# Optimization experiments

Measured on AMD Instinct MI355X. Metric: run time of the kernel, lower is better.

Reference implementation:

```python
import jax, jax.numpy as jnp
import numpy as np

NUM_USERS = 100_000
NUM_ITEMS = 50_000
DIM = 64
N_INTERACTIONS = 2_000_000  # symmetric nnz = 4M


def setup_inputs() -> dict:
    rng = np.random.default_rng(0)
    u = rng.integers(0, NUM_USERS, N_INTERACTIONS)
    it = rng.integers(0, NUM_ITEMS, N_INTERACTIONS) + NUM_USERS  # items offset by num_users
    rows = np.concatenate([u, it]).astype(np.int32)  # symmetric adjacency
    cols = np.concatenate([it, u]).astype(np.int32)
    n_nodes = NUM_USERS + NUM_ITEMS
    deg = np.bincount(rows, minlength=n_nodes).astype(np.float32)
    deg = np.maximum(deg, 1.0)
    # LightGCN symmetric normalization: A_hat[i,j] = 1/sqrt(deg_i * deg_j)
    vals = (1.0 / np.sqrt(deg[rows] * deg[cols])).astype(np.float32)

    key = jax.random.key(0)
    k1, k2 = jax.random.split(key)
    user_emb = jax.random.normal(k1, (NUM_USERS, DIM), jnp.float32) * 0.1
    item_emb = jax.random.normal(k2, (NUM_ITEMS, DIM), jnp.float32) * 0.1
    return {
        "user_emb": user_emb,
        "item_emb": item_emb,
        "rows": jnp.asarray(rows),
        "cols": jnp.asarray(cols),
        "vals": jnp.asarray(vals),
        "n_layers": 3,
    }


def reference(user_emb, item_emb, rows, cols, vals, n_layers):
    num_users = user_emb.shape[0]
    n_nodes = num_users + item_emb.shape[0]
    emb = jnp.concatenate([user_emb, item_emb], axis=0)  # [N, D]
    acc = emb
    cur = emb
    for _ in range(n_layers):
        # SpMM: cur = A_hat @ cur, via edge gather + weighted segment reduction
        msgs = vals[:, None] * cur[cols]  # [nnz, D]
        cur = jax.ops.segment_sum(msgs, rows, num_segments=n_nodes)
        acc = acc + cur
    all_emb = acc / (n_layers + 1)  # mean over [e0, e1, ..., eL]
    return all_emb[:num_users], all_emb[num_users:]
```

## Files before the change

### kernel.cpp

```cpp
#include <hip/hip_runtime.h>
#include <hip/hip_fp16.h>

#define D 64
#define NLAYERS 3
#define CHUNK 8192
#define RPB 256
#define NBMAX 640
#define NCHMAX 512
#define STAGE_CAP 8704

__global__ void init_concat(const float* __restrict__ ue, const float* __restrict__ ie,
                            const float* __restrict__ invsq,
                            __half* __restrict__ w0, float* __restrict__ acc,
                            int n_user_elems, int n_total_elems) {
    int i4 = (blockIdx.x * blockDim.x + threadIdx.x) * 4;
    if (i4 >= n_total_elems) return;
    float4 v;
    if (i4 < n_user_elems) v = *(const float4*)(ue + i4);
    else                   v = *(const float4*)(ie + (i4 - n_user_elems));
    *(float4*)(acc + i4) = v;
    float isr = invsq[i4 >> 6];
    __half2 h01 = __floats2half2_rn(isr * v.x, isr * v.y);
    __half2 h23 = __floats2half2_rn(isr * v.z, isr * v.w);
    float2 packed;
    *(__half2*)&packed.x = h01;
    *(__half2*)&packed.y = h23;
    *(float2*)(w0 + i4) = packed;
}

__global__ void partition_edges(const int* __restrict__ rows, const int* __restrict__ cols,
                                int* __restrict__ gsorted, int* __restrict__ goff_c,
                                int nnz, int nb) {
    __shared__ int staged[CHUNK];
    __shared__ int cnt[NBMAX];
    __shared__ int cur[NBMAX];
    __shared__ int partial[256];
    int t = threadIdx.x;
    int base = blockIdx.x * CHUNK;

    for (int j = t; j <= nb; j += 256) cnt[j] = 0;
    __syncthreads();
    for (int k = 0; k < CHUNK; k += 256) {
        int e = base + k + t;
        if (e < nnz) atomicAdd(&cnt[rows[e] >> 8], 1);
    }
    __syncthreads();
    int i0 = t * 3, i1 = i0 + 1, i2 = i0 + 2;
    int v0 = (i0 < nb) ? cnt[i0] : 0;
    int v1 = (i1 < nb) ? cnt[i1] : 0;
    int v2 = (i2 < nb) ? cnt[i2] : 0;
    partial[t] = v0 + v1 + v2;
    __syncthreads();
    for (int off = 1; off < 256; off <<= 1) {
        int x = (t >= off) ? partial[t - off] : 0;
        __syncthreads();
        partial[t] += x;
        __syncthreads();
    }
    int excl = (t == 0) ? 0 : partial[t - 1];
    if (i0 <= nb) cnt[i0] = excl;
    if (i1 <= nb) cnt[i1] = excl + v0;
    if (i2 <= nb) cnt[i2] = excl + v0 + v1;
    __syncthreads();
    for (int j = t; j < nb; j += 256) cur[j] = cnt[j];
    __syncthreads();
    for (int k = 0; k < CHUNK; k += 256) {
        int e = base + k + t;
        if (e < nnz) {
            int r = rows[e];
            int pos = atomicAdd(&cur[r >> 8], 1);
            staged[pos] = ((r & 255) << 18) | cols[e];
        }
    }
    __syncthreads();
    int total = cnt[nb];
    for (int i = t; i < total; i += 256) gsorted[base + i] = staged[i];
    for (int j = t; j <= nb; j += 256) goff_c[blockIdx.x * (nb + 1) + j] = cnt[j];
}

__global__ void transpose_off(const int* __restrict__ goff_c, int* __restrict__ T,
                              int nch, int nbp1) {
    int c = blockIdx.x * 256 + threadIdx.x;
    int j = blockIdx.y;
    if (c < nch) T[j * nch + c] = goff_c[c * nbp1 + j];
}

__global__ void bucket_totals(const int* __restrict__ T, int* __restrict__ btot, int nch) {
    int b = blockIdx.x;
    int lane = threadIdx.x;
    int s = 0;
    for (int c = lane; c < nch; c += 64)
        s += T[(size_t)(b + 1) * nch + c] - T[(size_t)b * nch + c];
    for (int off = 32; off; off >>= 1) s += __shfl_down(s, off, 64);
    if (lane == 0) btot[b] = s;
}

__global__ void scan_buckets(const int* __restrict__ btot, int* __restrict__ bb,
                             int* __restrict__ rp, int nb, int n_nodes, int nnz) {
    __shared__ int partial[256];
    int t = threadIdx.x;
    int i0 = t * 3, i1 = i0 + 1, i2 = i0 + 2;
    int v0 = (i0 < nb) ? btot[i0] : 0;
    int v1 = (i1 < nb) ? btot[i1] : 0;
    int v2 = (i2 < nb) ? btot[i2] : 0;
    partial[t] = v0 + v1 + v2;
    __syncthreads();
    for (int off = 1; off < 256; off <<= 1) {
        int x = (t >= off) ? partial[t - off] : 0;
        __syncthreads();
        partial[t] += x;
        __syncthreads();
    }
    int excl = (t == 0) ? 0 : partial[t - 1];
    if (i0 <= nb) bb[i0] = excl;
    if (i1 <= nb) bb[i1] = excl + v0;
    if (i2 <= nb) bb[i2] = excl + v0 + v1;
    if (t == 0) rp[n_nodes] = nnz;
}

__global__ __launch_bounds__(256)
void csr_build_bucket(const int* __restrict__ T, const int* __restrict__ gsorted,
                      const int* __restrict__ bb,
                      int* __restrict__ rp, float* __restrict__ invsq,
                      int* __restrict__ ci, int nch, int n_nodes) {
    __shared__ int staged[STAGE_CAP];
    __shared__ int sbeg[NCHMAX];
    __shared__ int slen[NCHMAX];
    __shared__ int soff[NCHMAX];
    __shared__ int cnt[RPB];
    __shared__ int cursor[RPB];
    __shared__ int scanb[256];
    int t = threadIdx.x;
    int b = blockIdx.x;
    for (int j = t; j < nch; j += 256) {
        int s0 = T[(size_t)b * nch + j];
        int s1 = T[(size_t)(b + 1) * nch + j];
        sbeg[j] = s0;
        slen[j] = s1 - s0;
    }
    cnt[t] = 0;
    __syncthreads();
    int i0 = 2 * t, i1 = 2 * t + 1;
    int l0 = (i0 < nch) ? slen[i0] : 0;
    int l1 = (i1 < nch) ? slen[i1] : 0;
    scanb[t] = l0 + l1;
    __syncthreads();
    for (int off = 1; off < 256; off <<= 1) {
        int x = (t >= off) ? scanb[t - off] : 0;
        __syncthreads();
        scanb[t] += x;
        __syncthreads();
    }
    int texcl = scanb[t] - (l0 + l1);
    if (i0 < nch) soff[i0] = texcl;
    if (i1 < nch) soff[i1] = texcl + l0;
    int total = scanb[255];
    __syncthreads();

    int w = t >> 6, lane = t & 63;
    int sub = lane >> 4, l16 = lane & 15;
    bool fits = (total <= STAGE_CAP);
    if (fits) {
        for (int c = (w << 2) + sub; c < nch; c += 16) {
            const int* seg = gsorted + (size_t)c * CHUNK + sbeg[c];
            int L = slen[c], o = soff[c];
            for (int i = l16; i < L; i += 16) staged[o + i] = seg[i];
        }
        __syncthreads();
        for (int i = t; i < total; i += 256) atomicAdd(&cnt[staged[i] >> 18], 1);
    } else {
        for (int c = (w << 2) + sub; c < nch; c += 16) {
            const int* seg = gsorted + (size_t)c * CHUNK + sbeg[c];
            int L = slen[c];
            for (int i = l16; i < L; i += 16) atomicAdd(&cnt[seg[i] >> 18], 1);
        }
    }
    __syncthreads();
    int v = cnt[t];
    scanb[t] = v;
    __syncthreads();
    for (int off = 1; off < 256; off <<= 1) {
        int x = (t >= off) ? scanb[t - off] : 0;
        __syncthreads();
        scanb[t] += x;
        __syncthreads();
    }
    int excl = scanb[t] - v;
    int base = bb[b];
    int grow = (b << 8) + t;
    if (grow < n_nodes) {
        rp[grow] = base + excl;
        float d = (float)v;
        invsq[grow] = rsqrtf(d < 1.f ? 1.f : d);
    }
    cursor[t] = base + excl;
    __syncthreads();
    if (fits) {
        for (int i = t; i < total; i += 256) {
            int p = staged[i];
            int pos = atomicAdd(&cursor[p >> 18], 1);
            ci[pos] = p & 0x3FFFF;
        }
    } else {
        for (int c = (w << 2) + sub; c < nch; c += 16) {
            const int* seg = gsorted + (size_t)c * CHUNK + sbeg[c];
            int L = slen[c];
            for (int i = l16; i < L; i += 16) {
                int p = seg[i];
                int pos = atomicAdd(&cursor[p >> 18], 1);
                ci[pos] = p & 0x3FFFF;
            }
        }
    }
}

__global__ void spmm_gather(const int* __restrict__ rp, const int* __restrict__ ci,
                            const __half* __restrict__ xh, const float* __restrict__ invsq,
                            __half* __restrict__ ynext, float* __restrict__ acc,
                            int row_beg, int row_end, int last) {
    int wid  = row_beg + ((blockIdx.x * blockDim.x + threadIdx.x) >> 6);
    int lane = threadIdx.x & 63;
    if (wid >= row_end) return;
    int sub = lane >> 4;
    int d4  = (lane & 15) << 2;
    int beg = rp[wid], end = rp[wid + 1];

    __half2 z = __floats2half2_rn(0.f, 0.f);
    __half2 a01 = z, a23 = z, b01 = z, b23 = z;
    int e = beg + sub;
    for (; e + 4 < end; e += 8) {
        int c0 = ci[e];
        int c1 = ci[e + 4];
        float2 r0 = *(const float2*)(xh + ((size_t)c0 << 6) + d4);
        float2 r1 = *(const float2*)(xh + ((size_t)c1 << 6) + d4);
        a01 = __hadd2(a01, *(__half2*)&r0.x);
        a23 = __hadd2(a23, *(__half2*)&r0.y);
        b01 = __hadd2(b01, *(__half2*)&r1.x);
        b23 = __hadd2(b23, *(__half2*)&r1.y);
    }
    if (e < end) {
        int c0 = ci[e];
        float2 r0 = *(const float2*)(xh + ((size_t)c0 << 6) + d4);
        a01 = __hadd2(a01, *(__half2*)&r0.x);
        a23 = __hadd2(a23, *(__half2*)&r0.y);
    }
    float2 fa01 = __half22float2(a01), fb01 = __half22float2(b01);
    float2 fa23 = __half22float2(a23), fb23 = __half22float2(b23);
    float4 s;
    s.x = fa01.x + fb01.x; s.y = fa01.y + fb01.y;
    s.z = fa23.x + fb23.x; s.w = fa23.y + fb23.y;
    s.x += __shfl_xor(s.x, 16, 64); s.y += __shfl_xor(s.y, 16, 64);
    s.z += __shfl_xor(s.z, 16, 64); s.w += __shfl_xor(s.w, 16, 64);
    s.x += __shfl_xor(s.x, 32, 64); s.y += __shfl_xor(s.y, 32, 64);
    s.z += __shfl_xor(s.z, 32, 64); s.w += __shfl_xor(s.w, 32, 64);

    if (sub == 0) {
        float isr = invsq[wid];
        float4 c4;
        c4.x = isr * s.x; c4.y = isr * s.y; c4.z = isr * s.z; c4.w = isr * s.w;
        size_t o = ((size_t)wid << 6) + d4;
        float4 a = *(float4*)(acc + o);
        if (last) {
            a.x = (a.x + c4.x) * 0.25f; a.y = (a.y + c4.y) * 0.25f;
            a.z = (a.z + c4.z) * 0.25f; a.w = (a.w + c4.w) * 0.25f;
            *(float4*)(acc + o) = a;
        } else {
            a.x += c4.x; a.y += c4.y; a.z += c4.z; a.w += c4.w;
            *(float4*)(acc + o) = a;
            __half2 h01 = __floats2half2_rn(isr * c4.x, isr * c4.y);
            __half2 h23 = __floats2half2_rn(isr * c4.z, isr * c4.w);
            float2 packed;
            *(__half2*)&packed.x = h01;
            *(__half2*)&packed.y = h23;
            *(float2*)(ynext + o) = packed;
        }
    }
}

extern "C" void kernel_launch(void* const* d_in, const int* in_sizes, int n_in,
                              void* d_out, int out_size, void* d_ws, size_t ws_size,
                              hipStream_t stream) {
    const float* ue   = (const float*)d_in[0];
    const float* ie   = (const float*)d_in[1];
    const int*   rows = (const int*)d_in[2];
    const int*   cols = (const int*)d_in[3];

    const int n_user_elems  = in_sizes[0];
    const int n_total_elems = out_size;
    const int n_nodes       = n_total_elems / D;
    const int n_user        = n_user_elems / D;
    const int nnz           = in_sizes[2];

    const int nb  = (n_nodes + RPB - 1) / RPB;
    const int nch = (nnz + CHUNK - 1) / CHUNK;

    float* acc = (float*)d_out;

    char* w = (char*)d_ws;
    __half* w0h    = (__half*)w; w += (size_t)n_total_elems * 2;
    __half* w1h    = (__half*)w; w += (size_t)n_total_elems * 2;
    int*   gsorted = (int*)w;    w += (size_t)nch * CHUNK * 4;
    int*   ci      = (int*)w;    w += (size_t)nnz * 4;
    float* invsq   = (float*)w;  w += (size_t)n_nodes * 4;
    int*   rp      = (int*)w;    w += ((size_t)n_nodes + 16) * 4;
    int*   goff_c  = (int*)w;    w += (size_t)nch * (nb + 1) * 4;
    int*   Tt      = (int*)w;    w += (size_t)(nb + 1) * nch * 4;
    int*   btot    = (int*)w;    w += (size_t)(nb + 16) * 4;
    int*   bb      = (int*)w;    w += (size_t)(nb + 16) * 4;

    partition_edges<<<nch, 256, 0, stream>>>(rows, cols, gsorted, goff_c, nnz, nb);
    dim3 tg((nch + 255) / 256, nb + 1);
    transpose_off<<<tg, 256, 0, stream>>>(goff_c, Tt, nch, nb + 1);
    bucket_totals<<<nb, 64, 0, stream>>>(Tt, btot, nch);
    scan_buckets<<<1, 256, 0, stream>>>(btot, bb, rp, nb, n_nodes, nnz);
    csr_build_bucket<<<nb, 256, 0, stream>>>(Tt, gsorted, bb, rp, invsq, ci, nch, n_nodes);

    const int elem_blocks = (n_total_elems / 4 + 255) / 256;
    init_concat<<<elem_blocks, 256, 0, stream>>>(ue, ie, invsq, w0h, acc,
                                                 n_user_elems, n_total_elems);

    __half* cur = w0h;
    __half* nxt = w1h;
    const int ublocks = (n_user * 64 + 255) / 256;
    const int iblocks = ((n_nodes - n_user) * 64 + 255) / 256;
    for (int l = 0; l < NLAYERS; ++l) {
        int last = (l == NLAYERS - 1);
        spmm_gather<<<ublocks, 256, 0, stream>>>(rp, ci, cur, invsq, nxt, acc,
                                                 0, n_user, last);
        spmm_gather<<<iblocks, 256, 0, stream>>>(rp, ci, cur, invsq, nxt, acc,
                                                 n_user, n_nodes, last);
        __half* t = cur; cur = nxt; nxt = t;
    }
}
```

Measured before the change: 518.5 us.

## Drop fp32 accumulator traffic, rebuild final mean from fp16 layer buffers; unroll gather

The running fp32 accumulator is removed. Layers 0 and 1 now write only the fp16 scaled embedding for the next layer. The last layer rebuilds the mean from the original fp32 inputs, the two stored fp16 intermediate layers (rescaled by sqrt(deg)) and the current sum, then writes the output with a nontemporal store. The gather loop is also unrolled to four independent edge streams with nontemporal index loads. This cuts per-layer fp32 read-modify-write traffic and raises memory-level parallelism, at the cost of extra register pressure and the precision of fp16 intermediates in the final sum.

```diff
diff --git a/kernel.cpp b/kernel.cpp
--- a/kernel.cpp
+++ b/kernel.cpp
@@ -9,16 +9,17 @@
 #define NCHMAX 512
 #define STAGE_CAP 8704
 
+typedef float vfloat4 __attribute__((ext_vector_type(4)));
+
 __global__ void init_concat(const float* __restrict__ ue, const float* __restrict__ ie,
                             const float* __restrict__ invsq,
-                            __half* __restrict__ w0, float* __restrict__ acc,
+                            __half* __restrict__ w0,
                             int n_user_elems, int n_total_elems) {
     int i4 = (blockIdx.x * blockDim.x + threadIdx.x) * 4;
     if (i4 >= n_total_elems) return;
     float4 v;
     if (i4 < n_user_elems) v = *(const float4*)(ue + i4);
     else                   v = *(const float4*)(ie + (i4 - n_user_elems));
-    *(float4*)(acc + i4) = v;
     float isr = invsq[i4 >> 6];
     __half2 h01 = __floats2half2_rn(isr * v.x, isr * v.y);
     __half2 h23 = __floats2half2_rn(isr * v.z, isr * v.w);
@@ -214,61 +215,93 @@
     }
 }
 
-__global__ void spmm_gather(const int* __restrict__ rp, const int* __restrict__ ci,
-                            const __half* __restrict__ xh, const float* __restrict__ invsq,
-                            __half* __restrict__ ynext, float* __restrict__ acc,
-                            int row_beg, int row_end, int last) {
+__global__ __launch_bounds__(256)
+void spmm_gather(const int* __restrict__ rp, const int* __restrict__ ci,
+                 const __half* __restrict__ xh, const float* __restrict__ invsq,
+                 __half* __restrict__ ynext,
+                 const __half* __restrict__ opA,
+                 const float* __restrict__ e0,
+                 float* __restrict__ outp,
+                 int row_beg, int row_end, int last) {
     int wid  = row_beg + ((blockIdx.x * blockDim.x + threadIdx.x) >> 6);
     int lane = threadIdx.x & 63;
     if (wid >= row_end) return;
     int sub = lane >> 4;
     int d4  = (lane & 15) << 2;
     int beg = rp[wid], end = rp[wid + 1];
+    float isr = invsq[wid];
+
+    float4 b4;
+    float2 q1, q2;
+    if (last && sub == 0) {
+        size_t o = ((size_t)wid << 6) + d4;
+        b4 = *(const float4*)(e0 + o);
+        q1 = *(const float2*)(opA + o);
+        q2 = *(const float2*)(xh + o);
+    }
 
     __half2 z = __floats2half2_rn(0.f, 0.f);
     __half2 a01 = z, a23 = z, b01 = z, b23 = z;
+    __half2 c01 = z, c23 = z, d01 = z, d23 = z;
     int e = beg + sub;
+    for (; e + 12 < end; e += 16) {
+        int k0 = __builtin_nontemporal_load(ci + e);
+        int k1 = __builtin_nontemporal_load(ci + e + 4);
+        int k2 = __builtin_nontemporal_load(ci + e + 8);
+        int k3 = __builtin_nontemporal_load(ci + e + 12);
+        float2 r0 = *(const float2*)(xh + ((size_t)k0 << 6) + d4);
+        float2 r1 = *(const float2*)(xh + ((size_t)k1 << 6) + d4);
+        float2 r2 = *(const float2*)(xh + ((size_t)k2 << 6) + d4);
+        float2 r3 = *(const float2*)(xh + ((size_t)k3 << 6) + d4);
+        a01 = __hadd2(a01, *(__half2*)&r0.x); a23 = __hadd2(a23, *(__half2*)&r0.y);
+        b01 = __hadd2(b01, *(__half2*)&r1.x); b23 = __hadd2(b23, *(__half2*)&r1.y);
+        c01 = __hadd2(c01, *(__half2*)&r2.x); c23 = __hadd2(c23, *(__half2*)&r2.y);
+        d01 = __hadd2(d01, *(__half2*)&r3.x); d23 = __hadd2(d23, *(__half2*)&r3.y);
+    }
     for (; e + 4 < end; e += 8) {
-        int c0 = ci[e];
-        int c1 = ci[e + 4];
-        float2 r0 = *(const float2*)(xh + ((size_t)c0 << 6) + d4);
-        float2 r1 = *(const float2*)(xh + ((size_t)c1 << 6) + d4);
-        a01 = __hadd2(a01, *(__half2*)&r0.x);
-        a23 = __hadd2(a23, *(__half2*)&r0.y);
-        b01 = __hadd2(b01, *(__half2*)&r1.x);
-        b23 = __hadd2(b23, *(__half2*)&r1.y);
+        int k0 = __builtin_nontemporal_load(ci + e);
+        int k1 = __builtin_nontemporal_load(ci + e + 4);
+        float2 r0 = *(const float2*)(xh + ((size_t)k0 << 6) + d4);
+        float2 r1 = *(const float2*)(xh + ((size_t)k1 << 6) + d4);
+        a01 = __hadd2(a01, *(__half2*)&r0.x); a23 = __hadd2(a23, *(__half2*)&r0.y);
+        b01 = __hadd2(b01, *(__half2*)&r1.x); b23 = __hadd2(b23, *(__half2*)&r1.y);
     }
     if (e < end) {
-        int c0 = ci[e];
-        float2 r0 = *(const float2*)(xh + ((size_t)c0 << 6) + d4);
-        a01 = __hadd2(a01, *(__half2*)&r0.x);
-        a23 = __hadd2(a23, *(__half2*)&r0.y);
-    }
-    float2 fa01 = __half22float2(a01), fb01 = __half22float2(b01);
-    float2 fa23 = __half22float2(a23), fb23 = __half22float2(b23);
-    float4 s;
-    s.x = fa01.x + fb01.x; s.y = fa01.y + fb01.y;
-    s.z = fa23.x + fb23.x; s.w = fa23.y + fb23.y;
-    s.x += __shfl_xor(s.x, 16, 64); s.y += __shfl_xor(s.y, 16, 64);
-    s.z += __shfl_xor(s.z, 16, 64); s.w += __shfl_xor(s.w, 16, 64);
-    s.x += __shfl_xor(s.x, 32, 64); s.y += __shfl_xor(s.y, 32, 64);
-    s.z += __shfl_xor(s.z, 32, 64); s.w += __shfl_xor(s.w, 32, 64);
+        int k0 = ci[e];
+        float2 r0 = *(const float2*)(xh + ((size_t)k0 << 6) + d4);
+        a01 = __hadd2(a01, *(__half2*)&r0.x); a23 = __hadd2(a23, *(__half2*)&r0.y);
+    }
+    float2 fa = __half22float2(a01), fb = __half22float2(b01);
+    float2 fc = __half22float2(c01), fd = __half22float2(d01);
+    float sx = (fa.x + fb.x) + (fc.x + fd.x);
+    float sy = (fa.y + fb.y) + (fc.y + fd.y);
+    fa = __half22float2(a23); fb = __half22float2(b23);
+    fc = __half22float2(c23); fd = __half22float2(d23);
+    float sz = (fa.x + fb.x) + (fc.x + fd.x);
+    float sw = (fa.y + fb.y) + (fc.y + fd.y);
+    sx += __shfl_xor(sx, 16, 64); sy += __shfl_xor(sy, 16, 64);
+    sz += __shfl_xor(sz, 16, 64); sw += __shfl_xor(sw, 16, 64);
+    sx += __shfl_xor(sx, 32, 64); sy += __shfl_xor(sy, 32, 64);
+    sz += __shfl_xor(sz, 32, 64); sw += __shfl_xor(sw, 32, 64);
 
     if (sub == 0) {
-        float isr = invsq[wid];
-        float4 c4;
-        c4.x = isr * s.x; c4.y = isr * s.y; c4.z = isr * s.z; c4.w = isr * s.w;
         size_t o = ((size_t)wid << 6) + d4;
-        float4 a = *(float4*)(acc + o);
+        float cx = isr * sx, cy = isr * sy, cz = isr * sz, cw = isr * sw;
         if (last) {
-            a.x = (a.x + c4.x) * 0.25f; a.y = (a.y + c4.y) * 0.25f;
-            a.z = (a.z + c4.z) * 0.25f; a.w = (a.w + c4.w) * 0.25f;
-            *(float4*)(acc + o) = a;
+            float sd = 1.0f / isr;
+            float2 f1a = __half22float2(*(__half2*)&q1.x);
+            float2 f1b = __half22float2(*(__half2*)&q1.y);
+            float2 f2a = __half22float2(*(__half2*)&q2.x);
+            float2 f2b = __half22float2(*(__half2*)&q2.y);
+            vfloat4 o4;
+            o4.x = (b4.x + (f1a.x + f2a.x) * sd + cx) * 0.25f;
+            o4.y = (b4.y + (f1a.y + f2a.y) * sd + cy) * 0.25f;
+            o4.z = (b4.z + (f1b.x + f2b.x) * sd + cz) * 0.25f;
+            o4.w = (b4.w + (f1b.y + f2b.y) * sd + cw) * 0.25f;
+            __builtin_nontemporal_store(o4, (vfloat4*)(outp + o));
         } else {
-            a.x += c4.x; a.y += c4.y; a.z += c4.z; a.w += c4.w;
-            *(float4*)(acc + o) = a;
-            __half2 h01 = __floats2half2_rn(isr * c4.x, isr * c4.y);
-            __half2 h23 = __floats2half2_rn(isr * c4.z, isr * c4.w);
+            __half2 h01 = __floats2half2_rn(isr * cx, isr * cy);
+            __half2 h23 = __floats2half2_rn(isr * cz, isr * cw);
             float2 packed;
             *(__half2*)&packed.x = h01;
             *(__half2*)&packed.y = h23;
@@ -294,7 +327,7 @@
     const int nb  = (n_nodes + RPB - 1) / RPB;
     const int nch = (nnz + CHUNK - 1) / CHUNK;
 
-    float* acc = (float*)d_out;
+    float* out = (float*)d_out;
 
     char* w = (char*)d_ws;
     __half* w0h    = (__half*)w; w += (size_t)n_total_elems * 2;
@@ -316,19 +349,21 @@
     csr_build_bucket<<<nb, 256, 0, stream>>>(Tt, gsorted, bb, rp, invsq, ci, nch, n_nodes);
 
     const int elem_blocks = (n_total_elems / 4 + 255) / 256;
-    init_concat<<<elem_blocks, 256, 0, stream>>>(ue, ie, invsq, w0h, acc,
+    init_concat<<<elem_blocks, 256, 0, stream>>>(ue, ie, invsq, w0h,
                                                  n_user_elems, n_total_elems);
 
+    const float* e0u = ue;
+    const float* e0i = ie - (size_t)n_user * D;
     __half* cur = w0h;
     __half* nxt = w1h;
     const int ublocks = (n_user * 64 + 255) / 256;
     const int iblocks = ((n_nodes - n_user) * 64 + 255) / 256;
     for (int l = 0; l < NLAYERS; ++l) {
         int last = (l == NLAYERS - 1);
-        spmm_gather<<<ublocks, 256, 0, stream>>>(rp, ci, cur, invsq, nxt, acc,
-                                                 0, n_user, last);
-        spmm_gather<<<iblocks, 256, 0, stream>>>(rp, ci, cur, invsq, nxt, acc,
-                                                 n_user, n_nodes, last);
+        spmm_gather<<<ublocks, 256, 0, stream>>>(rp, ci, cur, invsq, nxt,
+                                                 w1h, e0u, out, 0, n_user, last);
+        spmm_gather<<<iblocks, 256, 0, stream>>>(rp, ci, cur, invsq, nxt,
+                                                 w1h, e0i, out, n_user, n_nodes, last);
         __half* t = cur; cur = nxt; nxt = t;
     }
 }
```

After: 503.6 us. 2.9% less time.
